# Kernel tuning notes

Hardware: AMD Instinct MI355X
Metric: run time of the kernel (lower is better)

The kernel has to match this reference:

```python
import jax, jax.numpy as jnp
import numpy as np

WS = (2, 7, 7)  # window size (T, H, W)
NUM_HEADS = 8


def _relative_position_index():
    t, h, w = WS
    coords = np.stack(np.meshgrid(np.arange(t), np.arange(h), np.arange(w), indexing='ij'))  # (3,t,h,w)
    flat = coords.reshape(3, -1)  # (3, N)
    rel = flat[:, :, None] - flat[:, None, :]  # (3, N, N)
    rel = rel.transpose(1, 2, 0).astype(np.int32)  # (N, N, 3)
    rel[..., 0] += t - 1
    rel[..., 1] += h - 1
    rel[..., 2] += w - 1
    rel[..., 0] *= (2 * h - 1) * (2 * w - 1)
    rel[..., 1] *= 2 * w - 1
    return rel.sum(-1)  # (N, N)


def setup_inputs() -> dict:
    key = jax.random.key(0)
    ks = jax.random.split(key, 7)
    B_, N, C = 2048, 98, 256
    nW = 512
    table_size = (2 * WS[0] - 1) * (2 * WS[1] - 1) * (2 * WS[2] - 1)  # 507
    return {
        'x': jax.random.normal(ks[0], (B_, N, C), jnp.float32),
        'mask': jax.random.normal(ks[1], (nW, N, N), jnp.float32),
        'qkv_w': jax.random.normal(ks[2], (3 * C, C), jnp.float32) * 0.02,
        'qkv_b': jax.random.normal(ks[3], (3 * C,), jnp.float32) * 0.02,
        'proj_w': jax.random.normal(ks[4], (C, C), jnp.float32) * 0.02,
        'proj_b': jax.random.normal(ks[5], (C,), jnp.float32) * 0.02,
        'bias_table': jax.random.normal(ks[6], (table_size, NUM_HEADS), jnp.float32) * 0.02,
        'rel_index': jnp.asarray(_relative_position_index()),
    }


def reference(x, mask, qkv_w, qkv_b, proj_w, proj_b, bias_table, rel_index):
    B_, N, C = x.shape
    H = NUM_HEADS
    hd = C // H
    scale = hd ** -0.5
    # QKV projection -> (3, B_, H, N, hd)
    qkv = (x @ qkv_w.T + qkv_b).reshape(B_, N, 3, H, hd).transpose(2, 0, 3, 1, 4)
    q, k, v = qkv[0], qkv[1], qkv[2]
    attn = jnp.einsum('bhnd,bhmd->bhnm', q * scale, k)  # (B_, H, N, N)
    # gathered relative-position bias -> (H, N, N)
    bias = bias_table[rel_index.reshape(-1)].reshape(N, N, H).transpose(2, 0, 1)
    attn = attn + bias[None]
    nW = mask.shape[0]
    attn = attn.reshape(B_ // nW, nW, H, N, N) + mask[None, :, None]
    attn = jax.nn.softmax(attn.reshape(B_, H, N, N), axis=-1)
    out = jnp.einsum('bhnm,bhmd->bhnd', attn, v)  # (B_, H, N, hd)
    out = out.transpose(0, 2, 1, 3).reshape(B_, N, C)
    return out @ proj_w.T + proj_b
```

## Files before the change

kernel.cpp:

```cpp
#include <hip/hip_runtime.h>
#include <hip/hip_bf16.h>

typedef __attribute__((ext_vector_type(8))) short short8;
typedef __attribute__((ext_vector_type(4))) float f32x4;

__device__ __forceinline__ unsigned short f2bf(float f) {
    __hip_bfloat16 h = __float2bfloat16(f);
    union { __hip_bfloat16 h; unsigned short u; } c; c.h = h; return c.u;
}

typedef __attribute__((address_space(1))) const unsigned int gas_u32;
typedef __attribute__((address_space(3))) unsigned int las_u32;

__device__ __forceinline__ void gload_lds16(const unsigned short* g, unsigned short* l) {
    __builtin_amdgcn_global_load_lds((gas_u32*)g, (las_u32*)l, 16, 0, 0);
}

__global__ void cvt_bf16_kernel(const float* __restrict__ src,
                                unsigned short* __restrict__ dst, long n8) {
    long stride = (long)gridDim.x * 256;
    for (long t = (long)blockIdx.x * 256 + threadIdx.x; t < n8; t += stride) {
        long i = t * 8;
        float4 f0 = *reinterpret_cast<const float4*>(src + i);
        float4 f1 = *reinterpret_cast<const float4*>(src + i + 4);
        uint4 u;
        u.x = ((unsigned)f2bf(f0.y) << 16) | f2bf(f0.x);
        u.y = ((unsigned)f2bf(f0.w) << 16) | f2bf(f0.z);
        u.z = ((unsigned)f2bf(f1.y) << 16) | f2bf(f1.x);
        u.w = ((unsigned)f2bf(f1.w) << 16) | f2bf(f1.z);
        *reinterpret_cast<uint4*>(dst + i) = u;
    }
}

__global__ void mask_pad_kernel(const float* __restrict__ mask,
                                float* __restrict__ mask_pad) {
    int idx = blockIdx.x * 256 + threadIdx.x;
    if (idx >= 512 * 12544) return;
    int w = idx / 12544, rem = idx - w * 12544;
    int n = rem / 112, m = rem - n * 112;
    float v;
    if (m >= 98) v = -1e30f;
    else if (n >= 98) v = 0.f;
    else v = mask[w * 9604 + n * 98 + m];
    mask_pad[idx] = v;
}

__global__ void bias_pad_kernel(const float* __restrict__ bias_table,
                                const int* __restrict__ rel_index,
                                float* __restrict__ bias_pad) {
    int idx = blockIdx.x * 256 + threadIdx.x;
    if (idx >= 8 * 12544) return;
    int h = idx / 12544, rem = idx - h * 12544;
    int n = rem / 112, m = rem - n * 112;
    float v = (n < 98 && m < 98) ? bias_table[rel_index[n * 98 + m] * 8 + h] : 0.f;
    bias_pad[idx] = v;
}

__global__ void vt_zerofill_kernel(unsigned short* __restrict__ vtws) {
    int idx = blockIdx.x * 256 + threadIdx.x;
    if (idx >= 16384 * 32 * 7) return;
    int bhd = idx / 7, j = idx - bhd * 7;
    unsigned* p = reinterpret_cast<unsigned*>(vtws + (long)bhd * 112 + 98);
    p[j] = 0;
}

__global__ __launch_bounds__(256, 4)
void gemm_qkv_kernel(const unsigned short* __restrict__ Xb,
                     const unsigned short* __restrict__ Wb,
                     const float* __restrict__ bias,
                     unsigned short* __restrict__ qws,
                     unsigned short* __restrict__ kws,
                     unsigned short* __restrict__ vtws) {
    __shared__ unsigned short As[128 * 64];
    __shared__ unsigned short Bs[128 * 64];
    const int tid = threadIdx.x;
    const int wave = tid >> 6, lane = tid & 63;
    const int q4 = lane >> 4, l16 = lane & 15;
    const int wr = wave >> 1, wc = wave & 1;

    const int nwg = gridDim.x * gridDim.y;
    const int bid = blockIdx.y * gridDim.x + blockIdx.x;
    const int swz = (bid & 7) * (nwg >> 3) + (bid >> 3);
    const int bx = swz % gridDim.x;
    const int by = swz / gridDim.x;

    const long m0 = (long)by * 128;
    const int n0 = bx * 128;

    const int srow = lane >> 3;
    const int scol = (lane & 7) << 3;

    f32x4 acc[4][4];
#pragma unroll
    for (int i = 0; i < 4; ++i)
#pragma unroll
        for (int j = 0; j < 4; ++j) acc[i][j] = (f32x4){0.f, 0.f, 0.f, 0.f};

    for (int ks = 0; ks < 256; ks += 64) {
#pragma unroll
        for (int i = 0; i < 4; ++i) {
            int c = wave * 4 + i;
            gload_lds16(Xb + (m0 + c * 8 + srow) * 256 + ks + scol, &As[c * 512]);
            gload_lds16(Wb + (long)(n0 + c * 8 + srow) * 256 + ks + scol, &Bs[c * 512]);
        }
        __syncthreads();
#pragma unroll
        for (int s = 0; s < 2; ++s) {
            short8 a[4], b[4];
#pragma unroll
            for (int i = 0; i < 4; ++i)
                a[i] = *reinterpret_cast<const short8*>(&As[(wr * 64 + i * 16 + l16) * 64 + s * 32 + q4 * 8]);
#pragma unroll
            for (int j = 0; j < 4; ++j)
                b[j] = *reinterpret_cast<const short8*>(&Bs[(wc * 64 + j * 16 + l16) * 64 + s * 32 + q4 * 8]);
#pragma unroll
            for (int i = 0; i < 4; ++i)
#pragma unroll
                for (int j = 0; j < 4; ++j)
                    acc[i][j] = __builtin_amdgcn_mfma_f32_16x16x32_bf16(a[i], b[j], acc[i][j], 0, 0, 0);
        }
        __syncthreads();
    }
    const float scale = 0.17677669529663687f;
#pragma unroll
    for (int i = 0; i < 4; ++i) {
#pragma unroll
        for (int r = 0; r < 4; ++r) {
            long row = m0 + wr * 64 + i * 16 + q4 * 4 + r;
            int b_ = (int)(row / 98);
            int n_ = (int)(row - (long)b_ * 98);
#pragma unroll
            for (int j = 0; j < 4; ++j) {
                int col = n0 + wc * 64 + j * 16 + l16;
                float vv = acc[i][j][r] + bias[col];
                int which = col >> 8;
                int h = (col >> 5) & 7;
                int d = col & 31;
                if (which == 2) {
                    vtws[((long)(b_ * 8 + h) * 32 + d) * 112 + n_] = f2bf(vv);
                } else if (which == 1) {
                    kws[((long)(b_ * 8 + h) * 98 + n_) * 32 + d] = f2bf(vv);
                } else {
                    qws[((long)(b_ * 8 + h) * 98 + n_) * 32 + d] = f2bf(vv * scale);
                }
            }
        }
    }
}

__global__ __launch_bounds__(448, 7)
void attn_kernel(const unsigned short* __restrict__ q,
                 const unsigned short* __restrict__ k,
                 const unsigned short* __restrict__ vt,
                 const float* __restrict__ mask_pad,
                 const float* __restrict__ bias_pad,
                 unsigned short* __restrict__ attn_out) {
    __shared__ unsigned short Qs[112 * 40];
    __shared__ unsigned short Ks[112 * 40];
    __shared__ unsigned short Vt[32 * 136];

    const int tid = threadIdx.x;
    const int wave = tid >> 6, lane = tid & 63;
    const int q4 = lane >> 4, l16 = lane & 15;

    const int d0 = blockIdx.x;
    const int xcd = d0 & 7, jj = d0 >> 3;
    const int w = xcd * 64 + (jj >> 5);
    const int sub = jj & 31;
    const int b = (sub >> 3) * 512 + w;
    const int h = sub & 7;
    const int bh = b * 8 + h;
    const long base = (long)bh * 98 * 32;

    {
        int n = tid >> 2, dg = (tid & 3) * 8;
        uint4 vq = make_uint4(0, 0, 0, 0), vk = make_uint4(0, 0, 0, 0);
        if (n < 98) {
            vq = *reinterpret_cast<const uint4*>(q + base + n * 32 + dg);
            vk = *reinterpret_cast<const uint4*>(k + base + n * 32 + dg);
        }
        *reinterpret_cast<uint4*>(&Qs[n * 40 + dg]) = vq;
        *reinterpret_cast<uint4*>(&Ks[n * 40 + dg]) = vk;
    }
    {
        const unsigned short* vtp = vt + (long)bh * 3584;
        int d = tid / 14, ch = tid - d * 14;
        *reinterpret_cast<uint4*>(&Vt[d * 136 + ch * 8]) =
            *reinterpret_cast<const uint4*>(vtp + d * 112 + ch * 8);
    }
    if (tid < 64) {
        int d = tid >> 1, c = tid & 1;
        *reinterpret_cast<uint4*>(&Vt[d * 136 + 112 + c * 8]) = make_uint4(0, 0, 0, 0);
    }
    __syncthreads();

    const float* mp = mask_pad + (long)w * 12544;
    const float* bp = bias_pad + (long)h * 12544;
    const long obase = (long)b * 98 * 256 + h * 32;

    const int tr = wave;
    const int n = tr * 16 + l16;
    const float* mrow = mp + n * 112;
    const float* brow = bp + n * 112;
    short8 bq = *reinterpret_cast<const short8*>(&Qs[n * 40 + q4 * 8]);
    f32x4 pv[7];
#pragma unroll
    for (int i = 0; i < 7; ++i) {
        short8 ak = *reinterpret_cast<const short8*>(&Ks[(i * 16 + l16) * 40 + q4 * 8]);
        f32x4 d = (f32x4){0.f, 0.f, 0.f, 0.f};
        d = __builtin_amdgcn_mfma_f32_16x16x32_bf16(ak, bq, d, 0, 0, 0);
        int m0 = i * 16 + q4 * 4;
        float4 mk = *reinterpret_cast<const float4*>(mrow + m0);
        float4 bb = *reinterpret_cast<const float4*>(brow + m0);
        pv[i][0] = d[0] + mk.x + bb.x;
        pv[i][1] = d[1] + mk.y + bb.y;
        pv[i][2] = d[2] + mk.z + bb.z;
        pv[i][3] = d[3] + mk.w + bb.w;
    }
    float mx = -1e30f;
#pragma unroll
    for (int i = 0; i < 7; ++i)
#pragma unroll
        for (int r = 0; r < 4; ++r) mx = fmaxf(mx, pv[i][r]);
    mx = fmaxf(mx, __shfl_xor(mx, 16));
    mx = fmaxf(mx, __shfl_xor(mx, 32));
    float sm = 0.f;
#pragma unroll
    for (int i = 0; i < 7; ++i)
#pragma unroll
        for (int r = 0; r < 4; ++r) {
            float e = __expf(pv[i][r] - mx);
            pv[i][r] = e;
            sm += e;
        }
    sm += __shfl_xor(sm, 16);
    sm += __shfl_xor(sm, 32);
    float rinv = 1.f / sm;
    unsigned up[8][2];
#pragma unroll
    for (int i = 0; i < 7; ++i) {
        up[i][0] = ((unsigned)f2bf(pv[i][1] * rinv) << 16) | f2bf(pv[i][0] * rinv);
        up[i][1] = ((unsigned)f2bf(pv[i][3] * rinv) << 16) | f2bf(pv[i][2] * rinv);
    }
    up[7][0] = 0; up[7][1] = 0;
    f32x4 o0 = (f32x4){0.f, 0.f, 0.f, 0.f};
    f32x4 o1 = (f32x4){0.f, 0.f, 0.f, 0.f};
    const int srcA = ((q4 & 1) * 2) * 16 + l16;
    const int srcB = srcA + 16;
    const bool hi = (q4 >= 2);
#pragma unroll
    for (int kc = 0; kc < 4; ++kc) {
        int ie = 2 * kc, io = 2 * kc + 1;
        unsigned a0e = __shfl(up[ie][0], srcA), a0o = __shfl(up[io][0], srcA);
        unsigned a1e = __shfl(up[ie][1], srcA), a1o = __shfl(up[io][1], srcA);
        unsigned b0e = __shfl(up[ie][0], srcB), b0o = __shfl(up[io][0], srcB);
        unsigned b1e = __shfl(up[ie][1], srcB), b1o = __shfl(up[io][1], srcB);
        union { uint4 u; short8 s; } cvt;
        cvt.u.x = hi ? a0o : a0e;
        cvt.u.y = hi ? a1o : a1e;
        cvt.u.z = hi ? b0o : b0e;
        cvt.u.w = hi ? b1o : b1e;
        short8 bv0 = *reinterpret_cast<const short8*>(&Vt[l16 * 136 + kc * 32 + q4 * 8]);
        short8 bv1 = *reinterpret_cast<const short8*>(&Vt[(16 + l16) * 136 + kc * 32 + q4 * 8]);
        o0 = __builtin_amdgcn_mfma_f32_16x16x32_bf16(cvt.s, bv0, o0, 0, 0, 0);
        o1 = __builtin_amdgcn_mfma_f32_16x16x32_bf16(cvt.s, bv1, o1, 0, 0, 0);
    }
#pragma unroll
    for (int r = 0; r < 4; ++r) {
        int nn = tr * 16 + q4 * 4 + r;
        if (nn < 98) {
            attn_out[obase + nn * 256 + l16] = f2bf(o0[r]);
            attn_out[obase + nn * 256 + 16 + l16] = f2bf(o1[r]);
        }
    }
}

__global__ __launch_bounds__(256, 4)
void gemm_proj_kernel(const unsigned short* __restrict__ Abf,
                      const unsigned short* __restrict__ Wb,
                      const float* __restrict__ bias,
                      float* __restrict__ out) {
    __shared__ unsigned short As[128 * 64];
    __shared__ unsigned short Bs[128 * 64];
    const int tid = threadIdx.x;
    const int wave = tid >> 6, lane = tid & 63;
    const int q4 = lane >> 4, l16 = lane & 15;
    const int wr = wave >> 1, wc = wave & 1;

    const int nwg = gridDim.x * gridDim.y;
    const int bid = blockIdx.y * gridDim.x + blockIdx.x;
    const int swz = (bid & 7) * (nwg >> 3) + (bid >> 3);
    const int bx = swz % gridDim.x;
    const int by = swz / gridDim.x;

    const long m0 = (long)by * 128;
    const int n0 = bx * 128;

    const int srow = lane >> 3;
    const int scol = (lane & 7) << 3;

    f32x4 acc[4][4];
#pragma unroll
    for (int i = 0; i < 4; ++i)
#pragma unroll
        for (int j = 0; j < 4; ++j) acc[i][j] = (f32x4){0.f, 0.f, 0.f, 0.f};

    for (int ks = 0; ks < 256; ks += 64) {
#pragma unroll
        for (int i = 0; i < 4; ++i) {
            int c = wave * 4 + i;
            gload_lds16(Abf + (m0 + c * 8 + srow) * 256 + ks + scol, &As[c * 512]);
            gload_lds16(Wb + (long)(n0 + c * 8 + srow) * 256 + ks + scol, &Bs[c * 512]);
        }
        __syncthreads();
#pragma unroll
        for (int s = 0; s < 2; ++s) {
            short8 a[4], b[4];
#pragma unroll
            for (int i = 0; i < 4; ++i)
                a[i] = *reinterpret_cast<const short8*>(&As[(wr * 64 + i * 16 + l16) * 64 + s * 32 + q4 * 8]);
#pragma unroll
            for (int j = 0; j < 4; ++j)
                b[j] = *reinterpret_cast<const short8*>(&Bs[(wc * 64 + j * 16 + l16) * 64 + s * 32 + q4 * 8]);
#pragma unroll
            for (int i = 0; i < 4; ++i)
#pragma unroll
                for (int j = 0; j < 4; ++j)
                    acc[i][j] = __builtin_amdgcn_mfma_f32_16x16x32_bf16(a[i], b[j], acc[i][j], 0, 0, 0);
        }
        __syncthreads();
    }
#pragma unroll
    for (int i = 0; i < 4; ++i) {
#pragma unroll
        for (int r = 0; r < 4; ++r) {
            long row = m0 + wr * 64 + i * 16 + q4 * 4 + r;
#pragma unroll
            for (int j = 0; j < 4; ++j) {
                int col = n0 + wc * 64 + j * 16 + l16;
                out[row * 256 + col] = acc[i][j][r] + bias[col];
            }
        }
    }
}

extern "C" void kernel_launch(void* const* d_in, const int* in_sizes, int n_in,
                              void* d_out, int out_size, void* d_ws, size_t ws_size,
                              hipStream_t stream) {
    (void)in_sizes; (void)n_in; (void)out_size; (void)ws_size;
    const float* x          = (const float*)d_in[0];
    const float* mask       = (const float*)d_in[1];
    const float* qkv_w      = (const float*)d_in[2];
    const float* qkv_b      = (const float*)d_in[3];
    const float* proj_w     = (const float*)d_in[4];
    const float* proj_b     = (const float*)d_in[5];
    const float* bias_table = (const float*)d_in[6];
    const int*   rel_index  = (const int*)d_in[7];
    float* out = (float*)d_out;

    const long QN = 51380224;
    const long VT = 58720256;
    unsigned short* qws  = (unsigned short*)d_ws;
    unsigned short* kws  = qws + QN;
    unsigned short* vtws = kws + QN;
    unsigned short* aow  = vtws + VT;
    float* mask_padw = (float*)(aow + QN);
    float* bias_padw = mask_padw + 512 * 12544;
    unsigned short* wqkvb  = (unsigned short*)(bias_padw + 8 * 12544);
    unsigned short* wprojb = wqkvb + 768 * 256;
    unsigned short* xb = aow;

    vt_zerofill_kernel<<<dim3((16384 * 32 * 7 + 255) / 256), dim3(256), 0, stream>>>(vtws);
    mask_pad_kernel<<<dim3((512 * 12544 + 255) / 256), dim3(256), 0, stream>>>(
        mask, mask_padw);
    bias_pad_kernel<<<dim3((8 * 12544 + 255) / 256), dim3(256), 0, stream>>>(
        bias_table, rel_index, bias_padw);
    cvt_bf16_kernel<<<dim3(2048), dim3(256), 0, stream>>>(x, xb, 51380224L / 8);
    cvt_bf16_kernel<<<dim3(96), dim3(256), 0, stream>>>(qkv_w, wqkvb, 196608L / 8);
    cvt_bf16_kernel<<<dim3(32), dim3(256), 0, stream>>>(proj_w, wprojb, 65536L / 8);
    gemm_qkv_kernel<<<dim3(6, 1568), dim3(256), 0, stream>>>(
        xb, wqkvb, qkv_b, qws, kws, vtws);
    attn_kernel<<<dim3(16384), dim3(448), 0, stream>>>(
        qws, kws, vtws, mask_padw, bias_padw, aow);
    gemm_proj_kernel<<<dim3(2, 1568), dim3(256), 0, stream>>>(
        aow, wprojb, proj_b, out);
}
```

Measured before the change: 922.1 us.

## Stage QKV GEMM epilogue through LDS and store V untransposed

The QKV GEMM epilogue now writes bias-added, scaled bf16 results into shared memory, then emits coalesced 16-byte stores in head-major layout for Q, K and V alike. Previously each lane did scattered 2-byte stores, and V was transposed element by element into global memory. The attention kernel now transposes V into LDS itself and zero-fills the padding, which removes the separate zero-fill kernel and shrinks the V workspace. In exchange the attention load phase does scalar LDS scatter writes that may bank-conflict, and the GEMM uses more shared memory, which could lower occupancy.

```diff
diff --git a/kernel.cpp b/kernel.cpp
--- a/kernel.cpp
+++ b/kernel.cpp
@@ -56,23 +56,16 @@
     bias_pad[idx] = v;
 }
 
-__global__ void vt_zerofill_kernel(unsigned short* __restrict__ vtws) {
-    int idx = blockIdx.x * 256 + threadIdx.x;
-    if (idx >= 16384 * 32 * 7) return;
-    int bhd = idx / 7, j = idx - bhd * 7;
-    unsigned* p = reinterpret_cast<unsigned*>(vtws + (long)bhd * 112 + 98);
-    p[j] = 0;
-}
-
 __global__ __launch_bounds__(256, 4)
 void gemm_qkv_kernel(const unsigned short* __restrict__ Xb,
                      const unsigned short* __restrict__ Wb,
                      const float* __restrict__ bias,
                      unsigned short* __restrict__ qws,
                      unsigned short* __restrict__ kws,
-                     unsigned short* __restrict__ vtws) {
-    __shared__ unsigned short As[128 * 64];
-    __shared__ unsigned short Bs[128 * 64];
+                     unsigned short* __restrict__ vws) {
+    __shared__ unsigned short sh[17408];
+    unsigned short* As = sh;
+    unsigned short* Bs = sh + 8192;
     const int tid = threadIdx.x;
     const int wave = tid >> 6, lane = tid & 63;
     const int q4 = lane >> 4, l16 = lane & 15;
@@ -121,37 +114,45 @@
         }
         __syncthreads();
     }
-    const float scale = 0.17677669529663687f;
+
+    const float scale = (n0 < 256) ? 0.17677669529663687f : 1.0f;
 #pragma unroll
     for (int i = 0; i < 4; ++i) {
 #pragma unroll
-        for (int r = 0; r < 4; ++r) {
-            long row = m0 + wr * 64 + i * 16 + q4 * 4 + r;
-            int b_ = (int)(row / 98);
-            int n_ = (int)(row - (long)b_ * 98);
-#pragma unroll
-            for (int j = 0; j < 4; ++j) {
-                int col = n0 + wc * 64 + j * 16 + l16;
-                float vv = acc[i][j][r] + bias[col];
-                int which = col >> 8;
-                int h = (col >> 5) & 7;
-                int d = col & 31;
-                if (which == 2) {
-                    vtws[((long)(b_ * 8 + h) * 32 + d) * 112 + n_] = f2bf(vv);
-                } else if (which == 1) {
-                    kws[((long)(b_ * 8 + h) * 98 + n_) * 32 + d] = f2bf(vv);
-                } else {
-                    qws[((long)(b_ * 8 + h) * 98 + n_) * 32 + d] = f2bf(vv * scale);
-                }
+        for (int j = 0; j < 4; ++j) {
+            int c = wc * 64 + j * 16 + l16;
+            float bcol = bias[n0 + c];
+#pragma unroll
+            for (int r = 0; r < 4; ++r) {
+                int row = wr * 64 + i * 16 + q4 * 4 + r;
+                sh[row * 136 + c] = f2bf((acc[i][j][r] + bcol) * scale);
             }
         }
+    }
+    __syncthreads();
+
+    const int whichb = n0 >> 8;
+    unsigned short* dstm = (whichb == 0) ? qws : ((whichb == 1) ? kws : vws);
+    const int cbase = n0 & 255;
+#pragma unroll
+    for (int it = 0; it < 8; ++it) {
+        int id = it * 256 + tid;
+        int m = id >> 4;
+        int ch = id & 15;
+        uint4 u = *reinterpret_cast<const uint4*>(&sh[m * 136 + ch * 8]);
+        long row = m0 + m;
+        int b_ = (int)(row / 98);
+        int n_ = (int)(row - (long)b_ * 98);
+        int c = cbase + ch * 8;
+        int h = c >> 5, d0 = c & 31;
+        *reinterpret_cast<uint4*>(dstm + (((long)(b_ * 8 + h) * 98 + n_) * 32 + d0)) = u;
     }
 }
 
 __global__ __launch_bounds__(448, 7)
 void attn_kernel(const unsigned short* __restrict__ q,
                  const unsigned short* __restrict__ k,
-                 const unsigned short* __restrict__ vt,
+                 const unsigned short* __restrict__ v,
                  const float* __restrict__ mask_pad,
                  const float* __restrict__ bias_pad,
                  unsigned short* __restrict__ attn_out) {
@@ -163,8 +164,8 @@
     const int wave = tid >> 6, lane = tid & 63;
     const int q4 = lane >> 4, l16 = lane & 15;
 
-    const int d0 = blockIdx.x;
-    const int xcd = d0 & 7, jj = d0 >> 3;
+    const int d0_ = blockIdx.x;
+    const int xcd = d0_ & 7, jj = d0_ >> 3;
     const int w = xcd * 64 + (jj >> 5);
     const int sub = jj & 31;
     const int b = (sub >> 3) * 512 + w;
@@ -182,15 +183,18 @@
         *reinterpret_cast<uint4*>(&Qs[n * 40 + dg]) = vq;
         *reinterpret_cast<uint4*>(&Ks[n * 40 + dg]) = vk;
     }
+    for (int i = tid; i < 32 * 30; i += 448) {
+        int d = i / 30, nn = 98 + (i - d * 30);
+        Vt[d * 136 + nn] = 0;
+    }
     {
-        const unsigned short* vtp = vt + (long)bh * 3584;
-        int d = tid / 14, ch = tid - d * 14;
-        *reinterpret_cast<uint4*>(&Vt[d * 136 + ch * 8]) =
-            *reinterpret_cast<const uint4*>(vtp + d * 112 + ch * 8);
-    }
-    if (tid < 64) {
-        int d = tid >> 1, c = tid & 1;
-        *reinterpret_cast<uint4*>(&Vt[d * 136 + 112 + c * 8]) = make_uint4(0, 0, 0, 0);
+        int n = tid >> 2, d0 = (tid & 3) * 8;
+        if (n < 98) {
+            union { uint4 u; unsigned short e[8]; } cvt;
+            cvt.u = *reinterpret_cast<const uint4*>(v + base + n * 32 + d0);
+#pragma unroll
+            for (int kk = 0; kk < 8; ++kk) Vt[(d0 + kk) * 136 + n] = cvt.e[kk];
+        }
     }
     __syncthreads();
 
@@ -359,18 +363,16 @@
     float* out = (float*)d_out;
 
     const long QN = 51380224;
-    const long VT = 58720256;
     unsigned short* qws  = (unsigned short*)d_ws;
     unsigned short* kws  = qws + QN;
-    unsigned short* vtws = kws + QN;
-    unsigned short* aow  = vtws + VT;
+    unsigned short* vws  = kws + QN;
+    unsigned short* aow  = vws + QN;
     float* mask_padw = (float*)(aow + QN);
     float* bias_padw = mask_padw + 512 * 12544;
     unsigned short* wqkvb  = (unsigned short*)(bias_padw + 8 * 12544);
     unsigned short* wprojb = wqkvb + 768 * 256;
     unsigned short* xb = aow;
 
-    vt_zerofill_kernel<<<dim3((16384 * 32 * 7 + 255) / 256), dim3(256), 0, stream>>>(vtws);
     mask_pad_kernel<<<dim3((512 * 12544 + 255) / 256), dim3(256), 0, stream>>>(
         mask, mask_padw);
     bias_pad_kernel<<<dim3((8 * 12544 + 255) / 256), dim3(256), 0, stream>>>(
@@ -379,9 +381,9 @@
     cvt_bf16_kernel<<<dim3(96), dim3(256), 0, stream>>>(qkv_w, wqkvb, 196608L / 8);
     cvt_bf16_kernel<<<dim3(32), dim3(256), 0, stream>>>(proj_w, wprojb, 65536L / 8);
     gemm_qkv_kernel<<<dim3(6, 1568), dim3(256), 0, stream>>>(
-        xb, wqkvb, qkv_b, qws, kws, vtws);
+        xb, wqkvb, qkv_b, qws, kws, vws);
     attn_kernel<<<dim3(16384), dim3(448), 0, stream>>>(
-        qws, kws, vtws, mask_padw, bias_padw, aow);
+        qws, kws, vws, mask_padw, bias_padw, aow);
     gemm_proj_kernel<<<dim3(2, 1568), dim3(256), 0, stream>>>(
         aow, wprojb, proj_b, out);
 }
```

Result: faster. 825.1 us (-10.5%).
